# Optimization experiments

Hardware: AMD Instinct MI355X
Metric: run time of the kernel (lower is better)

Reference implementation:

```python
import jax, jax.numpy as jnp
import numpy as np

N = 200000   # nodes
E = 800000   # edges
G = 10000    # graphs in batch
H = 128      # hidden_channels
IN_NODE = 26  # 10-2 + 16 + 2
IN_EDGE = 13  # 4-3 + 8 + 2*2


def setup_inputs() -> dict:
    key = jax.random.key(0)
    ks = jax.random.split(key, 30)
    f = lambda i, shape: (jax.random.normal(ks[i], shape, jnp.float32) * 0.1)
    inp = {}
    inp['atom_num'] = jax.random.randint(ks[0], (N,), 0, 119)
    inp['atom_arom'] = jax.random.randint(ks[1], (N,), 0, 2)
    inp['x_cont'] = f(2, (N, 8))
    inp['bond_type'] = jax.random.randint(ks[3], (E,), 0, 22)
    inp['edge_cont'] = f(4, (E, 1))
    inp['bond_conj'] = jax.random.randint(ks[5], (E,), 0, 2)
    inp['bond_arom'] = jax.random.randint(ks[6], (E,), 0, 2)
    inp['edge_index'] = jax.random.randint(ks[7], (2, E), 0, N)
    inp['batch'] = jnp.sort(jax.random.randint(ks[8], (N,), 0, G))
    # embeddings (padding rows zeroed, matching padding_idx)
    inp['atom_emb'] = f(9, (119, 16)).at[0].set(0.0)
    inp['bond_emb'] = f(10, (22, 8)).at[0].set(0.0)
    inp['bool_emb'] = f(11, (3, 2)).at[2].set(0.0)
    # GATv2 layer 1 (gnn1)
    inp['Wl1'] = f(12, (IN_NODE, H)); inp['bl1'] = f(13, (H,))
    inp['Wr1'] = f(14, (IN_NODE, H)); inp['br1'] = f(15, (H,))
    inp['We1'] = f(16, (IN_EDGE, H))
    inp['att1'] = f(17, (H,)); inp['bias1'] = f(18, (H,))
    # GATv2 shared layer (gnn) -- used for layers 2 and 3 with the SAME weights
    inp['Wl2'] = f(19, (H, H)); inp['bl2'] = f(20, (H,))
    inp['Wr2'] = f(21, (H, H)); inp['br2'] = f(22, (H,))
    inp['We2'] = f(23, (IN_EDGE, H))
    inp['att2'] = f(24, (H,)); inp['bias2'] = f(25, (H,))
    return inp


def _gatv2(x, src, dst, ea, Wl, bl, Wr, br, We, att, bias):
    """PyG GATv2Conv, heads=1, add_self_loops=True, fill_value='mean'."""
    n = x.shape[0]
    # self-loop edge features = mean of incoming edge features per node
    deg = jax.ops.segment_sum(jnp.ones((src.shape[0],), x.dtype), dst, num_segments=n)
    ea_mean = jax.ops.segment_sum(ea, dst, num_segments=n) / jnp.clip(deg, 1.0)[:, None]
    loop = jnp.arange(n, dtype=src.dtype)
    s = jnp.concatenate([src, loop])
    d = jnp.concatenate([dst, loop])
    ea_full = jnp.concatenate([ea, ea_mean], axis=0)
    xl = x @ Wl + bl   # source transform
    xr = x @ Wr + br   # destination transform
    m = xl[s] + xr[d] + ea_full @ We           # [E+N, H]
    m = jax.nn.leaky_relu(m, 0.2)
    logits = m @ att                            # [E+N]
    mx = jax.ops.segment_max(logits, d, num_segments=n)
    a = jnp.exp(logits - mx[d])
    denom = jax.ops.segment_sum(a, d, num_segments=n)
    alpha = a / denom[d]
    out = jax.ops.segment_sum(alpha[:, None] * xl[s], d, num_segments=n)
    return out + bias


def reference(atom_num, atom_arom, x_cont, bond_type, edge_cont, bond_conj,
              bond_arom, edge_index, batch, atom_emb, bond_emb, bool_emb,
              Wl1, bl1, Wr1, br1, We1, att1, bias1,
              Wl2, bl2, Wr2, br2, We2, att2, bias2):
    src, dst = edge_index[0], edge_index[1]
    x = jnp.concatenate([atom_emb[atom_num], x_cont, bool_emb[atom_arom]], axis=1)  # [N,26]
    ea = jnp.concatenate([bond_emb[bond_type], edge_cont,
                          bool_emb[bond_conj], bool_emb[bond_arom]], axis=1)        # [E,13]
    h = jax.nn.relu(_gatv2(x, src, dst, ea, Wl1, bl1, Wr1, br1, We1, att1, bias1))
    # num_layers_gnn=3 -> shared-weight layer applied twice (dropout off in eval)
    h = jax.nn.relu(_gatv2(h, src, dst, ea, Wl2, bl2, Wr2, br2, We2, att2, bias2))
    h = jax.nn.relu(_gatv2(h, src, dst, ea, Wl2, bl2, Wr2, br2, We2, att2, bias2))
    pooled = jax.ops.segment_max(h, batch, num_segments=G)  # global_max_pool
    pooled = jnp.where(jnp.isfinite(pooled), pooled, 0.0)   # guard empty graphs
    return pooled
```

## Files before the change

kernel.cpp:

```cpp
#include <hip/hip_runtime.h>
#include <hip/hip_bf16.h>
#include <cstdint>
#include <cstdio>


typedef __attribute__((ext_vector_type(8))) short bf16x8;
typedef __attribute__((ext_vector_type(8))) unsigned short u16x8;
typedef __attribute__((ext_vector_type(4))) float f32x4;

#define TBT_S 132

static __device__ __forceinline__ float leaky02(float v) { return v > 0.f ? v : 0.2f * v; }
static __device__ __forceinline__ float b2f(unsigned short u) {
    return __uint_as_float(((unsigned)u) << 16);
}
static __device__ __forceinline__ unsigned short f2b(float f) {
    __hip_bfloat16 h = __float2bfloat16(f);
    return *(unsigned short*)&h;
}


__global__ __launch_bounds__(256) void prep_init(
    int* __restrict__ degcnt, int n_degcnt,
    int* __restrict__ outz, int n_out,
    const float* __restrict__ Wl2, const float* __restrict__ Wr2,
    __hip_bfloat16* __restrict__ Wp,
    const float* __restrict__ Wl1, const float* __restrict__ Wr1,
    __hip_bfloat16* __restrict__ Wp1,
    const int* __restrict__ atom_num, const int* __restrict__ atom_arom,
    const float* __restrict__ x_cont, const float* __restrict__ atom_emb,
    const float* __restrict__ bool_emb, __hip_bfloat16* __restrict__ Xf, int N,
    int e_z1, int e_z2, int e_pw, int e_pw1)
{
    int b = blockIdx.x;
    if (b < e_z1) {
        int i = b * 256 + threadIdx.x;
        if (i < n_degcnt) degcnt[i] = 0;
    } else if (b < e_z2) {
        int i = (b - e_z1) * 256 + threadIdx.x;
        if (i < n_out) outz[i] = 0;
    } else if (b < e_pw) {
        int idx = (b - e_z2) * 256 + threadIdx.x;
        int j    = idx & 7;
        int lane = (idx >> 3) & 63;
        int ks   = (idx >> 9) & 3;
        int nt   = idx >> 11;
        int k = ks * 32 + ((lane >> 4) << 3) + j;
        int n = nt * 16 + (lane & 15);
        float v = (n < 128) ? Wl2[k * 128 + n] : Wr2[k * 128 + (n - 128)];
        Wp[idx] = __float2bfloat16(v);
    } else if (b < e_pw1) {
        int idx = (b - e_pw) * 256 + threadIdx.x;
        int j    = idx & 7;
        int lane = (idx >> 3) & 63;
        int ntc  = idx >> 9;
        int k = ((lane >> 4) << 3) + j;
        int n = ntc * 16 + (lane & 15);
        float v = 0.f;
        if (k < 26) v = (n < 128) ? Wl1[k * 128 + n] : Wr1[k * 128 + (n - 128)];
        Wp1[idx] = __float2bfloat16(v);
    } else {
        int n = (b - e_pw1) * 256 + threadIdx.x;
        if (n >= N) return;
        int an = atom_num[n], am = atom_arom[n];
        unsigned short v[32];
#pragma unroll
        for (int k = 0; k < 16; k++) v[k] = f2b(atom_emb[an * 16 + k]);
#pragma unroll
        for (int k = 0; k < 8; k++)  v[16 + k] = f2b(x_cont[(size_t)n * 8 + k]);
        v[24] = f2b(bool_emb[am * 2]);
        v[25] = f2b(bool_emb[am * 2 + 1]);
#pragma unroll
        for (int k = 26; k < 32; k++) v[k] = 0;
        unsigned short* dst = (unsigned short*)Xf + (size_t)n * 32;
#pragma unroll
        for (int q = 0; q < 4; q++)
            *(u16x8*)(dst + q * 8) = *(const u16x8*)&v[q * 8];
    }
}


__global__ __launch_bounds__(256) void count_deg(
    const int* __restrict__ dst, int* __restrict__ deg, int E)
{
    int e = blockIdx.x * 256 + threadIdx.x;
    if (e < E) atomicAdd(&deg[dst[e]], 1);
}

#define SORT_BLK 1024

__global__ __launch_bounds__(256) void sort_hist(
    const int* __restrict__ deg, int* __restrict__ block_hist, int N)
{
    __shared__ int h[512];
    for (int i = threadIdx.x; i < 512; i += 256) h[i] = 0;
    __syncthreads();
    int base = blockIdx.x * SORT_BLK;
#pragma unroll
    for (int k = 0; k < 4; k++) {
        int n = base + k * 256 + threadIdx.x;
        if (n < N) {
            int d = deg[n]; if (d > 511) d = 511;
            atomicAdd(&h[d], 1);
        }
    }
    __syncthreads();
    for (int i = threadIdx.x; i < 512; i += 256)
        block_hist[blockIdx.x * 512 + i] = h[i];
}

__global__ __launch_bounds__(512) void sort_scan(
    int* __restrict__ block_hist, int* __restrict__ bin_base,
    int* __restrict__ edge_base, int nsb)
{
    __shared__ int s[512];
    int t = threadIdx.x;
    int acc = 0;
    for (int b = 0; b < nsb; b++) {
        int v = block_hist[b * 512 + t];
        block_hist[b * 512 + t] = acc;
        acc += v;
    }
    s[t] = acc;
    __syncthreads();
    for (int off = 1; off < 512; off <<= 1) {
        int x = (t >= off) ? s[t - off] : 0;
        __syncthreads();
        s[t] += x;
        __syncthreads();
    }
    bin_base[t] = s[t] - acc;
    __syncthreads();
    int ec = acc * t;
    s[t] = ec;
    __syncthreads();
    for (int off = 1; off < 512; off <<= 1) {
        int x = (t >= off) ? s[t - off] : 0;
        __syncthreads();
        s[t] += x;
        __syncthreads();
    }
    edge_base[t] = s[t] - ec;
}

__global__ __launch_bounds__(256) void sort_scatter(
    const int* __restrict__ deg, const int* __restrict__ block_hist,
    const int* __restrict__ bin_base, const int* __restrict__ edge_base,
    int4* __restrict__ meta, int* __restrict__ nrp, int N)
{
    __shared__ int h[512];
    for (int i = threadIdx.x; i < 512; i += 256) h[i] = 0;
    __syncthreads();
    int bs = blockIdx.x;
    int base = bs * SORT_BLK;
#pragma unroll
    for (int k = 0; k < 4; k++) {
        int n = base + k * 256 + threadIdx.x;
        if (n < N) {
            int d = deg[n]; if (d > 511) d = 511;
            int r = atomicAdd(&h[d], 1);
            int posInBin = block_hist[bs * 512 + d] + r;
            int pos = bin_base[d] + posInBin;
            int rp = edge_base[d] + posInBin * d;
            int4 m; m.x = rp; m.y = d; m.z = n; m.w = 0;
            meta[pos] = m;
            nrp[n] = rp;
        }
    }
}

__global__ __launch_bounds__(256) void csr_fill(
    const int* __restrict__ src, const int* __restrict__ dst,
    const int* __restrict__ bond_type, const float* __restrict__ edge_cont,
    const int* __restrict__ bond_conj, const int* __restrict__ bond_arom,
    const int* __restrict__ nrp, int* __restrict__ cnt,
    int4* __restrict__ csr_rec, int E)
{
    int e = blockIdx.x * 256 + threadIdx.x;
    if (e >= E) return;
    int d = dst[e];
    int pos = nrp[d] + atomicAdd(&cnt[d], 1);
    int codes = (bond_type[e] & 0xFF) | ((bond_conj[e] & 1) << 8) | ((bond_arom[e] & 1) << 16);
    int4 rec;
    rec.x = src[e];
    rec.y = codes;
    rec.z = __float_as_int(edge_cont[e]);
    rec.w = 0;
    csr_rec[pos] = rec;
}


__global__ __launch_bounds__(256) void gemm_mfma1(
    const __hip_bfloat16* __restrict__ Xf,
    const __hip_bfloat16* __restrict__ Wp,
    const float* __restrict__ bl, const float* __restrict__ br,
    __hip_bfloat16* __restrict__ XL, __hip_bfloat16* __restrict__ XR, int N)
{
    __shared__ unsigned short sT[64 * 256];
    int lane = threadIdx.x & 63;
    int wave = threadIdx.x >> 6;
    int row0 = blockIdx.x * 64;
    int m_lane = lane & 15;
    int quad = lane >> 4;
    const unsigned short* Xu = (const unsigned short*)Xf;
    const unsigned short* Wu = (const unsigned short*)Wp;

    f32x4 acc[4][4];
#pragma unroll
    for (int mt = 0; mt < 4; mt++)
#pragma unroll
        for (int nt = 0; nt < 4; nt++) acc[mt][nt] = (f32x4){0.f, 0.f, 0.f, 0.f};

    bf16x8 a[4], b[4];
#pragma unroll
    for (int mt = 0; mt < 4; mt++)
        a[mt] = *(const bf16x8*)(Xu + (size_t)(row0 + mt * 16 + m_lane) * 32 + quad * 8);
#pragma unroll
    for (int nt = 0; nt < 4; nt++)
        b[nt] = *(const bf16x8*)(Wu + ((wave * 4 + nt) * 64 + lane) * 8);
#pragma unroll
    for (int mt = 0; mt < 4; mt++)
#pragma unroll
        for (int nt = 0; nt < 4; nt++)
            acc[mt][nt] = __builtin_amdgcn_mfma_f32_16x16x32_bf16(
                a[mt], b[nt], acc[mt][nt], 0, 0, 0);

#pragma unroll
    for (int nt = 0; nt < 4; nt++) {
        int col = wave * 64 + nt * 16 + m_lane;
        float bv = (col < 128) ? bl[col] : br[col - 128];
#pragma unroll
        for (int mt = 0; mt < 4; mt++) {
            int rbase = mt * 16 + quad * 4;
#pragma unroll
            for (int reg = 0; reg < 4; reg++)
                sT[(rbase + reg) * 256 + col] = f2b(acc[mt][nt][reg] + bv);
        }
    }

    __syncthreads();

    unsigned short* XLu = (unsigned short*)XL;
    unsigned short* XRu = (unsigned short*)XR;
    int t = threadIdx.x;
#pragma unroll
    for (int q = 0; q < 4; q++) {
        int s = t * 32 + q * 8;
        int r = s >> 7, c = s & 127;
        *(u16x8*)(XLu + (size_t)(row0 + r) * 128 + c) = *(const u16x8*)&sT[r * 256 + c];
        *(u16x8*)(XRu + (size_t)(row0 + r) * 128 + c) = *(const u16x8*)&sT[r * 256 + 128 + c];
    }
}

__global__ __launch_bounds__(256) void gemm_mfma(
    const __hip_bfloat16* H,
    const __hip_bfloat16* __restrict__ Wp,
    const float* __restrict__ bl, const float* __restrict__ br,
    __hip_bfloat16* __restrict__ XL, __hip_bfloat16* XR, int N)
{
    __shared__ unsigned short sT[64 * 256];
    int lane = threadIdx.x & 63;
    int wave = threadIdx.x >> 6;
    int row0 = blockIdx.x * 64;
    int m_lane = lane & 15;
    int quad = lane >> 4;
    const unsigned short* Hu = (const unsigned short*)H;
    const unsigned short* Wu = (const unsigned short*)Wp;

    f32x4 acc[4][4];
#pragma unroll
    for (int mt = 0; mt < 4; mt++)
#pragma unroll
        for (int nt = 0; nt < 4; nt++) acc[mt][nt] = (f32x4){0.f, 0.f, 0.f, 0.f};

#pragma unroll
    for (int ks = 0; ks < 4; ks++) {
        int koff = ks * 32 + quad * 8;
        bf16x8 a[4], b[4];
#pragma unroll
        for (int mt = 0; mt < 4; mt++)
            a[mt] = *(const bf16x8*)(Hu + (size_t)(row0 + mt * 16 + m_lane) * 128 + koff);
#pragma unroll
        for (int nt = 0; nt < 4; nt++)
            b[nt] = *(const bf16x8*)(Wu + ((((wave * 4 + nt) * 4) + ks) * 64 + lane) * 8);
#pragma unroll
        for (int mt = 0; mt < 4; mt++)
#pragma unroll
            for (int nt = 0; nt < 4; nt++)
                acc[mt][nt] = __builtin_amdgcn_mfma_f32_16x16x32_bf16(
                    a[mt], b[nt], acc[mt][nt], 0, 0, 0);
    }

#pragma unroll
    for (int nt = 0; nt < 4; nt++) {
        int col = wave * 64 + nt * 16 + m_lane;
        float bv = (col < 128) ? bl[col] : br[col - 128];
#pragma unroll
        for (int mt = 0; mt < 4; mt++) {
            int rbase = mt * 16 + quad * 4;
#pragma unroll
            for (int reg = 0; reg < 4; reg++)
                sT[(rbase + reg) * 256 + col] = f2b(acc[mt][nt][reg] + bv);
        }
    }

    __syncthreads();

    unsigned short* XLu = (unsigned short*)XL;
    unsigned short* XRu = (unsigned short*)XR;
    int t = threadIdx.x;
#pragma unroll
    for (int q = 0; q < 4; q++) {
        int s = t * 32 + q * 8;
        int r = s >> 7, c = s & 127;
        *(u16x8*)(XLu + (size_t)(row0 + r) * 128 + c) = *(const u16x8*)&sT[r * 256 + c];
        *(u16x8*)(XRu + (size_t)(row0 + r) * 128 + c) = *(const u16x8*)&sT[r * 256 + 128 + c];
    }
}

__global__ __launch_bounds__(256) void gat_fused(
    const int4* __restrict__ meta, const int4* __restrict__ csr_rec,
    const float* __restrict__ bond_emb, const float* __restrict__ bool_emb,
    const __hip_bfloat16* __restrict__ XL, const __hip_bfloat16* XR,
    const float* __restrict__ We,
    const float* __restrict__ att,
    const float* __restrict__ bias,
    __hip_bfloat16* OUT, int N)
{
    __shared__ float sTbt[22 * TBT_S];
    __shared__ float sTca[4 * TBT_S];
    __shared__ float sW8[128];

    for (int i = threadIdx.x; i < 22 * 128; i += 256) {
        int bt = i >> 7, c = i & 127;
        float s = 0.f;
#pragma unroll
        for (int k = 0; k < 8; k++) s = fmaf(bond_emb[bt * 8 + k], We[k * 128 + c], s);
        sTbt[bt * TBT_S + c] = s;
    }
    for (int i = threadIdx.x; i < 4 * 128; i += 256) {
        int idx = i >> 7, c = i & 127;
        int cj = idx >> 1, ar = idx & 1;
        float s = bool_emb[cj * 2]     * We[9 * 128 + c]
                + bool_emb[cj * 2 + 1] * We[10 * 128 + c]
                + bool_emb[ar * 2]     * We[11 * 128 + c]
                + bool_emb[ar * 2 + 1] * We[12 * 128 + c];
        sTca[idx * TBT_S + c] = s;
    }
    if (threadIdx.x < 128) sW8[threadIdx.x] = We[8 * 128 + threadIdx.x];
    __syncthreads();

    int lane = threadIdx.x & 63;
    int wave = threadIdx.x >> 6;
    int sl   = lane & 15;
    int sw   = lane >> 4;
    int cbase = sl * 8;

    float a8[8], bs8[8], w88[8];
    {
        float4 t0 = *(const float4*)&att[cbase],  t1 = *(const float4*)&att[cbase + 4];
        float4 u0 = *(const float4*)&bias[cbase], u1 = *(const float4*)&bias[cbase + 4];
        float4 v0 = *(const float4*)&sW8[cbase],  v1 = *(const float4*)&sW8[cbase + 4];
#pragma unroll
        for (int i = 0; i < 4; i++) {
            a8[i] = (&t0.x)[i];  a8[i + 4] = (&t1.x)[i];
            bs8[i] = (&u0.x)[i]; bs8[i + 4] = (&u1.x)[i];
            w88[i] = (&v0.x)[i]; w88[i + 4] = (&v1.x)[i];
        }
    }

    const unsigned short* XLu = (const unsigned short*)XL;
    const unsigned short* XRu = (const unsigned short*)XR;
    unsigned short* OUTu = (unsigned short*)OUT;

    int group = (blockIdx.x * 4 + wave) * 4 + sw;
    int stride = gridDim.x * 16;
    for (int idx = group; idx < N; idx += stride) {
        int4 mt = meta[idx];
        int rp = mt.x, dg = mt.y, n = mt.z;
        u16x8 uxr = *(const u16x8*)(XRu + (size_t)n * 128 + cbase);
        float xr[8];
#pragma unroll
        for (int i = 0; i < 8; i++) xr[i] = b2f(uxr[i]);

        float runs = 0.f;
        float acc[8], ets[8];
#pragma unroll
        for (int i = 0; i < 8; i++) { acc[i] = 0.f; ets[i] = 0.f; }

        for (int j = 0; j < dg; j += 4) {
            int cnt = dg - j; if (cnt > 4) cnt = 4;
            int4 rec[4];
#pragma unroll
            for (int jj = 0; jj < 4; jj++)
                if (jj < cnt) rec[jj] = csr_rec[rp + j + jj];
            u16x8 uv[4];
#pragma unroll
            for (int jj = 0; jj < 4; jj++)
                if (jj < cnt)
                    uv[jj] = *(const u16x8*)(XLu + (size_t)rec[jj].x * 128 + cbase);

            float part[4];
#pragma unroll
            for (int jj = 0; jj < 4; jj++) {
                if (jj >= cnt) continue;
                int bt = rec[jj].y & 0xFF;
                int ca = (((rec[jj].y >> 8) & 1) << 1) | ((rec[jj].y >> 16) & 1);
                float ec = __int_as_float(rec[jj].z);
                const float* tb = &sTbt[bt * TBT_S + cbase];
                const float* tc = &sTca[ca * TBT_S + cbase];
                float p = 0.f;
#pragma unroll
                for (int i = 0; i < 8; i++) {
                    float et = fmaf(ec, w88[i], tb[i] + tc[i]);
                    ets[i] += et;
                    float m = leaky02(xr[i] + b2f(uv[jj][i]) + et);
                    p = fmaf(m, a8[i], p);
                }
                p += __shfl_xor(p, 1);
                p += __shfl_xor(p, 2);
                p += __shfl_xor(p, 4);
                p += __shfl_xor(p, 8);
                part[jj] = p;
            }
#pragma unroll
            for (int jj = 0; jj < 4; jj++) {
                if (jj >= cnt) continue;
                float wgt = __expf(part[jj]);
                runs += wgt;
#pragma unroll
                for (int i = 0; i < 8; i++)
                    acc[i] = fmaf(wgt, b2f(uv[jj][i]), acc[i]);
            }
        }

        {
            u16x8 un = *(const u16x8*)(XLu + (size_t)n * 128 + cbase);
            float invd = 1.f / (float)(dg > 0 ? dg : 1);
            float p = 0.f;
#pragma unroll
            for (int i = 0; i < 8; i++) {
                float m = leaky02(xr[i] + b2f(un[i]) + ets[i] * invd);
                p = fmaf(m, a8[i], p);
            }
            p += __shfl_xor(p, 1);
            p += __shfl_xor(p, 2);
            p += __shfl_xor(p, 4);
            p += __shfl_xor(p, 8);
            float wgt = __expf(p);
            runs += wgt;
#pragma unroll
            for (int i = 0; i < 8; i++)
                acc[i] = fmaf(wgt, b2f(un[i]), acc[i]);
        }

        float inv = 1.f / runs;
        u16x8 o;
#pragma unroll
        for (int i = 0; i < 8; i++)
            o[i] = f2b(fmaxf(fmaf(acc[i], inv, bs8[i]), 0.f));
        *(u16x8*)(OUTu + (size_t)n * 128 + cbase) = o;
    }
}

__global__ __launch_bounds__(128) void pool_max(
    const __hip_bfloat16* __restrict__ H, const int* __restrict__ batch,
    float* __restrict__ out, int N)
{
    int c = threadIdx.x;
    int n0 = blockIdx.x * 64;
    int nend = n0 + 64; if (nend > N) nend = N;
    const unsigned short* Hu = (const unsigned short*)H;
    int g_cur = -1;
    float acc = 0.f;
    for (int n = n0; n < nend; ++n) {
        int g = batch[n];
        if (g != g_cur) {
            if (g_cur >= 0)
                atomicMax((int*)out + (size_t)g_cur * 128 + c, __float_as_int(acc));
            g_cur = g;
            acc = 0.f;
        }
        acc = fmaxf(acc, b2f(Hu[(size_t)n * 128 + c]));
    }
    if (g_cur >= 0)
        atomicMax((int*)out + (size_t)g_cur * 128 + c, __float_as_int(acc));
}


static inline size_t align_up(size_t x, size_t a) { return (x + a - 1) & ~(a - 1); }
static inline int cdiv(int a, int b) { return (a + b - 1) / b; }

extern "C" void kernel_launch(void* const* d_in, const int* in_sizes, int n_in,
                              void* d_out, int out_size, void* d_ws, size_t ws_size,
                              hipStream_t stream)
{
    const int N = in_sizes[0];
    const int E = in_sizes[3];

    const int*   atom_num  = (const int*)d_in[0];
    const int*   atom_arom = (const int*)d_in[1];
    const float* x_cont    = (const float*)d_in[2];
    const int*   bond_type = (const int*)d_in[3];
    const float* edge_cont = (const float*)d_in[4];
    const int*   bond_conj = (const int*)d_in[5];
    const int*   bond_arom = (const int*)d_in[6];
    const int*   e_src     = (const int*)d_in[7];
    const int*   e_dst     = e_src + E;
    const int*   batch     = (const int*)d_in[8];
    const float* atom_emb  = (const float*)d_in[9];
    const float* bond_emb  = (const float*)d_in[10];
    const float* bool_emb  = (const float*)d_in[11];
    const float* Wl1 = (const float*)d_in[12]; const float* bl1 = (const float*)d_in[13];
    const float* Wr1 = (const float*)d_in[14]; const float* br1 = (const float*)d_in[15];
    const float* We1 = (const float*)d_in[16]; const float* att1 = (const float*)d_in[17];
    const float* bias1 = (const float*)d_in[18];
    const float* Wl2 = (const float*)d_in[19]; const float* bl2 = (const float*)d_in[20];
    const float* Wr2 = (const float*)d_in[21]; const float* br2 = (const float*)d_in[22];
    const float* We2 = (const float*)d_in[23]; const float* att2 = (const float*)d_in[24];
    const float* bias2 = (const float*)d_in[25];
    float* out = (float*)d_out;

    const int nsb = cdiv(N, SORT_BLK);

    char* w = (char*)d_ws;
    size_t off = 0;
    auto alloc = [&](size_t bytes) {
        void* p = w + off;
        off = align_up(off + bytes, 256);
        return p;
    };
    __hip_bfloat16* A  = (__hip_bfloat16*)alloc((size_t)N * 128 * 2);
    __hip_bfloat16* B  = (__hip_bfloat16*)alloc((size_t)N * 128 * 2);
    __hip_bfloat16* Xf = (__hip_bfloat16*)alloc((size_t)N * 32 * 2);
    __hip_bfloat16* Wp = (__hip_bfloat16*)alloc((size_t)32768 * 2);
    __hip_bfloat16* Wp1= (__hip_bfloat16*)alloc((size_t)8192 * 2);
    int*   degcnt  = (int*)alloc((size_t)2 * N * 4);
    int*   deg     = degcnt;
    int*   cnt     = degcnt + N;
    int4*  csr_rec = (int4*)alloc((size_t)E * 16);
    int4*  meta    = (int4*)alloc((size_t)N * 16);
    int*   nrp     = (int*)alloc((size_t)N * 4);
    int*   block_hist = (int*)alloc((size_t)nsb * 512 * 4);
    int*   bin_base   = (int*)alloc(512 * 4);
    int*   edge_base  = (int*)alloc(512 * 4);
    size_t required = off;

    fprintf(stderr, "[GNN] ws_size=%zu required=%zu%s\n", ws_size, required,
            ws_size < required ? "  INSUFFICIENT - skipping" : "");
    if (ws_size < required) return;

    int bz1 = cdiv(2 * N, 256);
    int bz2 = cdiv(out_size, 256);
    int bpw = 32768 / 256;
    int bpw1 = 8192 / 256;
    int bbx = cdiv(N, 256);
    int e_z1 = bz1, e_z2 = e_z1 + bz2, e_pw = e_z2 + bpw, e_pw1 = e_pw + bpw1;
    prep_init<<<e_pw1 + bbx, 256, 0, stream>>>(
        degcnt, 2 * N, (int*)out, out_size,
        Wl2, Wr2, Wp, Wl1, Wr1, Wp1,
        atom_num, atom_arom, x_cont, atom_emb, bool_emb, Xf, N,
        e_z1, e_z2, e_pw, e_pw1);

    count_deg<<<cdiv(E, 256), 256, 0, stream>>>(e_dst, deg, E);
    sort_hist<<<nsb, 256, 0, stream>>>(deg, block_hist, N);
    sort_scan<<<1, 512, 0, stream>>>(block_hist, bin_base, edge_base, nsb);
    sort_scatter<<<nsb, 256, 0, stream>>>(deg, block_hist, bin_base, edge_base,
                                          meta, nrp, N);
    csr_fill<<<cdiv(E, 256), 256, 0, stream>>>(e_src, e_dst, bond_type, edge_cont,
                                               bond_conj, bond_arom, nrp, cnt,
                                               csr_rec, E);

    const int fused_blocks = 1536;

    gemm_mfma1<<<N / 64, 256, 0, stream>>>(Xf, Wp1, bl1, br1, A, B, N);
    gat_fused<<<fused_blocks, 256, 0, stream>>>(
        meta, csr_rec, bond_emb, bool_emb, A, B, We1, att1, bias1, B, N);

    for (int layer = 0; layer < 2; ++layer) {
        gemm_mfma<<<N / 64, 256, 0, stream>>>(B, Wp, bl2, br2, A, B, N);
        gat_fused<<<fused_blocks, 256, 0, stream>>>(
            meta, csr_rec, bond_emb, bool_emb, A, B, We2, att2, bias2, B, N);
    }

    pool_max<<<cdiv(N, 64), 128, 0, stream>>>(B, batch, out, N);
}
```

Measured before the change: 721.6 us.

## Software-pipeline next node's metadata and edge records in GAT aggregation loop

The GAT aggregation loop now prefetches the next node's meta entry, its XR row and its first four CSR edge records while the current node is processed. The first edge chunk and the self-loop XL row are loaded up front, so the dependent metadata -> record -> XL gather chain overlaps with compute. It also adds a launch_bounds occupancy hint of 4 blocks. The cost is higher register pressure from the prefetched state, which could reduce occupancy or cause spills.

```diff
diff --git a/kernel.cpp b/kernel.cpp
--- a/kernel.cpp
+++ b/kernel.cpp
@@ -318,7 +318,7 @@
     }
 }
 
-__global__ __launch_bounds__(256) void gat_fused(
+__global__ __launch_bounds__(256, 4) void gat_fused(
     const int4* __restrict__ meta, const int4* __restrict__ csr_rec,
     const float* __restrict__ bond_emb, const float* __restrict__ bool_emb,
     const __hip_bfloat16* __restrict__ XL, const __hip_bfloat16* XR,
@@ -375,38 +375,58 @@
 
     int group = (blockIdx.x * 4 + wave) * 4 + sw;
     int stride = gridDim.x * 16;
+
+    int4 mt;
+    int4 recs[4];
+    u16x8 xru;
+    {
+        int safe = (group < N) ? group : 0;
+        mt = meta[safe];
+        xru = *(const u16x8*)(XRu + (size_t)mt.z * 128 + cbase);
+        int c0 = mt.y < 4 ? mt.y : 4;
+#pragma unroll
+        for (int jj = 0; jj < 4; jj++)
+            if (jj < c0) recs[jj] = csr_rec[mt.x + jj];
+    }
+
     for (int idx = group; idx < N; idx += stride) {
-        int4 mt = meta[idx];
         int rp = mt.x, dg = mt.y, n = mt.z;
-        u16x8 uxr = *(const u16x8*)(XRu + (size_t)n * 128 + cbase);
+        int cnt0 = dg < 4 ? dg : 4;
+
+        u16x8 uv[4];
+#pragma unroll
+        for (int jj = 0; jj < 4; jj++)
+            if (jj < cnt0)
+                uv[jj] = *(const u16x8*)(XLu + (size_t)recs[jj].x * 128 + cbase);
+        u16x8 un = *(const u16x8*)(XLu + (size_t)n * 128 + cbase);
+
+        int nidx = idx + stride;
+        int nsafe = (nidx < N) ? nidx : 0;
+        int4 mt_n = meta[nsafe];
+        u16x8 xru_n = *(const u16x8*)(XRu + (size_t)mt_n.z * 128 + cbase);
+        int4 recs_n[4];
+        int cn = mt_n.y < 4 ? mt_n.y : 4;
+#pragma unroll
+        for (int jj = 0; jj < 4; jj++)
+            if (jj < cn) recs_n[jj] = csr_rec[mt_n.x + jj];
+
         float xr[8];
 #pragma unroll
-        for (int i = 0; i < 8; i++) xr[i] = b2f(uxr[i]);
+        for (int i = 0; i < 8; i++) xr[i] = b2f(xru[i]);
 
         float runs = 0.f;
         float acc[8], ets[8];
 #pragma unroll
         for (int i = 0; i < 8; i++) { acc[i] = 0.f; ets[i] = 0.f; }
 
-        for (int j = 0; j < dg; j += 4) {
-            int cnt = dg - j; if (cnt > 4) cnt = 4;
-            int4 rec[4];
-#pragma unroll
-            for (int jj = 0; jj < 4; jj++)
-                if (jj < cnt) rec[jj] = csr_rec[rp + j + jj];
-            u16x8 uv[4];
-#pragma unroll
-            for (int jj = 0; jj < 4; jj++)
-                if (jj < cnt)
-                    uv[jj] = *(const u16x8*)(XLu + (size_t)rec[jj].x * 128 + cbase);
-
+        {
             float part[4];
 #pragma unroll
             for (int jj = 0; jj < 4; jj++) {
-                if (jj >= cnt) continue;
-                int bt = rec[jj].y & 0xFF;
-                int ca = (((rec[jj].y >> 8) & 1) << 1) | ((rec[jj].y >> 16) & 1);
-                float ec = __int_as_float(rec[jj].z);
+                if (jj >= cnt0) continue;
+                int bt = recs[jj].y & 0xFF;
+                int ca = (((recs[jj].y >> 8) & 1) << 1) | ((recs[jj].y >> 16) & 1);
+                float ec = __int_as_float(recs[jj].z);
                 const float* tb = &sTbt[bt * TBT_S + cbase];
                 const float* tc = &sTca[ca * TBT_S + cbase];
                 float p = 0.f;
@@ -425,17 +445,61 @@
             }
 #pragma unroll
             for (int jj = 0; jj < 4; jj++) {
+                if (jj >= cnt0) continue;
+                float wgt = __expf(part[jj]);
+                runs += wgt;
+#pragma unroll
+                for (int i = 0; i < 8; i++)
+                    acc[i] = fmaf(wgt, b2f(uv[jj][i]), acc[i]);
+            }
+        }
+
+        for (int j = 4; j < dg; j += 4) {
+            int cnt = dg - j; if (cnt > 4) cnt = 4;
+            int4 rec2[4];
+#pragma unroll
+            for (int jj = 0; jj < 4; jj++)
+                if (jj < cnt) rec2[jj] = csr_rec[rp + j + jj];
+            u16x8 uv2[4];
+#pragma unroll
+            for (int jj = 0; jj < 4; jj++)
+                if (jj < cnt)
+                    uv2[jj] = *(const u16x8*)(XLu + (size_t)rec2[jj].x * 128 + cbase);
+            float part[4];
+#pragma unroll
+            for (int jj = 0; jj < 4; jj++) {
+                if (jj >= cnt) continue;
+                int bt = rec2[jj].y & 0xFF;
+                int ca = (((rec2[jj].y >> 8) & 1) << 1) | ((rec2[jj].y >> 16) & 1);
+                float ec = __int_as_float(rec2[jj].z);
+                const float* tb = &sTbt[bt * TBT_S + cbase];
+                const float* tc = &sTca[ca * TBT_S + cbase];
+                float p = 0.f;
+#pragma unroll
+                for (int i = 0; i < 8; i++) {
+                    float et = fmaf(ec, w88[i], tb[i] + tc[i]);
+                    ets[i] += et;
+                    float m = leaky02(xr[i] + b2f(uv2[jj][i]) + et);
+                    p = fmaf(m, a8[i], p);
+                }
+                p += __shfl_xor(p, 1);
+                p += __shfl_xor(p, 2);
+                p += __shfl_xor(p, 4);
+                p += __shfl_xor(p, 8);
+                part[jj] = p;
+            }
+#pragma unroll
+            for (int jj = 0; jj < 4; jj++) {
                 if (jj >= cnt) continue;
                 float wgt = __expf(part[jj]);
                 runs += wgt;
 #pragma unroll
                 for (int i = 0; i < 8; i++)
-                    acc[i] = fmaf(wgt, b2f(uv[jj][i]), acc[i]);
+                    acc[i] = fmaf(wgt, b2f(uv2[jj][i]), acc[i]);
             }
         }
 
         {
-            u16x8 un = *(const u16x8*)(XLu + (size_t)n * 128 + cbase);
             float invd = 1.f / (float)(dg > 0 ? dg : 1);
             float p = 0.f;
 #pragma unroll
@@ -460,6 +524,11 @@
         for (int i = 0; i < 8; i++)
             o[i] = f2b(fmaxf(fmaf(acc[i], inv, bs8[i]), 0.f));
         *(u16x8*)(OUTu + (size_t)n * 128 + cbase) = o;
+
+        mt = mt_n;
+        xru = xru_n;
+#pragma unroll
+        for (int jj = 0; jj < 4; jj++) recs[jj] = recs_n[jj];
     }
 }
 
```

Result: slower. 1.396 ms (+93.5%).
